# Kernel optimization log

Measured on AMD Instinct MI355X. Metric: run time of the kernel, lower is better.

The kernel has to match this reference:

```python
import jax, jax.numpy as jnp
import numpy as np

D_MODEL = 512
NUM_HEADS = 8
HEAD_DIM = D_MODEL // NUM_HEADS  # 64
EMBEDDING_DIM = 512  # undefined global EmbeddingDim in source -> d_model
EVENT_DIM = 388      # undefined global EventDim in source -> MIDI event vocab
B, T = 2, 2048


def setup_inputs() -> dict:
    key = jax.random.key(0)
    ks = jax.random.split(key, 12)
    sc = 0.02
    v = jax.random.normal(ks[0], (B, T, D_MODEL), jnp.float32)
    k = jax.random.normal(ks[1], (B, T, D_MODEL), jnp.float32)
    q = jax.random.normal(ks[2], (B, T, D_MODEL), jnp.float32)
    mask = jnp.tril(jnp.ones((T, T), jnp.float32))  # causal mask, broadcasts to [H,B,T,T]
    Wq = jax.random.normal(ks[3], (D_MODEL, HEAD_DIM), jnp.float32) * sc
    bq = jnp.zeros((HEAD_DIM,), jnp.float32)
    Wk = jax.random.normal(ks[4], (D_MODEL, HEAD_DIM), jnp.float32) * sc
    bk = jnp.zeros((HEAD_DIM,), jnp.float32)
    Wv = jax.random.normal(ks[5], (D_MODEL, HEAD_DIM), jnp.float32) * sc
    bv = jnp.zeros((HEAD_DIM,), jnp.float32)
    E = jax.random.normal(ks[6], (NUM_HEADS, T, HEAD_DIM), jnp.float32) * sc
    Wo = jax.random.normal(ks[7], (D_MODEL, EMBEDDING_DIM), jnp.float32) * sc
    bo = jnp.zeros((EMBEDDING_DIM,), jnp.float32)
    Wl = jax.random.normal(ks[8], (EMBEDDING_DIM, EVENT_DIM), jnp.float32) * sc
    bl = jnp.zeros((EVENT_DIM,), jnp.float32)
    return {"v": v, "k": k, "q": q, "mask": mask, "Wq": Wq, "bq": bq,
            "Wk": Wk, "bk": bk, "Wv": Wv, "bv": bv, "E": E,
            "Wo": Wo, "bo": bo, "Wl": Wl, "bl": bl}


def _skew(S):
    # S: [H,B,T,T] -> Music-Transformer skew via left-pad, reshape, slice
    H, Bb, Tt, _ = S.shape
    S = jnp.pad(S, ((0, 0), (0, 0), (0, 0), (1, 0)))          # [H,B,T,T+1]
    S = S.reshape(H, Bb, Tt + 1, Tt)                           # [H,B,T+1,T]
    return S[:, :, 1:]                                         # [H,B,T,T]


def reference(v, k, q, mask, Wq, bq, Wk, bk, Wv, bv, E, Wo, bo, Wl, bl):
    # The source applies the SAME Dense per head, so all heads share q/k/v projections
    qh = q @ Wq + bq  # [B,T,hd]
    kh = k @ Wk + bk  # [B,T,hd]
    vh = v @ Wv + bv  # [B,T,hd]
    # relative-position scores per head: Q @ E^T then skew
    S = jnp.einsum('btd,hsd->hbts', qh, E)  # [H,B,T,T]
    S = _skew(S)
    qk = jnp.einsum('btd,bsd->bts', qh, kh)  # [B,T,T], identical across heads
    attn = (qk[None] + S) / np.sqrt(HEAD_DIM)  # [H,B,T,T]
    attn = attn * mask - jnp.asarray(1e10, attn.dtype) * (1.0 - mask)
    score = jax.nn.softmax(attn, axis=-1)
    ctx = jnp.einsum('hbts,bsd->hbtd', score, vh)  # [H,B,T,hd]
    ctx = jnp.transpose(ctx, (1, 2, 0, 3)).reshape(ctx.shape[1], ctx.shape[2], -1)  # [B,T,d_model]
    ctx = jax.nn.relu(ctx @ Wo + bo)  # [B,T,EmbeddingDim]
    logits = ctx @ Wl + bl            # [B,T,EventDim]
    return logits
```

## Files before the change

kernel.cpp:

```cpp
#include <hip/hip_runtime.h>
#include <hip/hip_bf16.h>


#define B_ 2
#define T_ 2048
#define DM_ 512
#define H_ 8
#define HD_ 64
#define ED_ 512
#define EV_ 388
#define BT_ (B_ * T_)

typedef __attribute__((ext_vector_type(8))) short short8;
typedef __attribute__((ext_vector_type(4))) float floatx4;

#define MFMA(a, b, c) __builtin_amdgcn_mfma_f32_16x16x32_bf16((a), (b), (c), 0, 0, 0)

__device__ __forceinline__ float bfs(unsigned short s) {
  union { unsigned int i; float f; } v; v.i = ((unsigned int)s) << 16; return v.f;
}
__device__ __forceinline__ unsigned short f2bf(float f) {
  __hip_bfloat16 h = __float2bfloat16(f);
  union { __hip_bfloat16 h; unsigned short u; } v; v.h = h; return v.u;
}
__device__ __forceinline__ float ldf(const void* p, int i, bool isbf) {
  return isbf ? bfs(((const unsigned short*)p)[i]) : ((const float*)p)[i];
}
__device__ __forceinline__ bool det_bf(const unsigned int* mask) {
  return mask[0] != 0x3F800000u;
}

__global__ __launch_bounds__(256) void prep_kernel(
    const void* __restrict__ E, const void* __restrict__ Wq,
    const void* __restrict__ Wk, const void* __restrict__ Wv,
    const void* __restrict__ Wo, const void* __restrict__ Wl,
    const unsigned int* __restrict__ mask,
    unsigned short* __restrict__ E_c, unsigned short* __restrict__ WqT,
    unsigned short* __restrict__ WkT, unsigned short* __restrict__ WvT,
    unsigned short* __restrict__ WoT, unsigned short* __restrict__ WlT) {
  const bool isbf = det_bf(mask);
  const int tid = threadIdx.x;
  int bi = blockIdx.x;
  if (bi < 1024) {
    const int i0 = (bi * 256 + tid) * 4;
    if (isbf) {
      *(uint2*)&E_c[i0] = *(const uint2*)((const unsigned short*)E + i0);
    } else {
      float4 f = *(const float4*)((const float*)E + i0);
      unsigned short p[4] = {f2bf(f.x), f2bf(f.y), f2bf(f.z), f2bf(f.w)};
      *(uint2*)&E_c[i0] = *(uint2*)p;
    }
    return;
  }
  bi -= 1024;
  const void* src; unsigned short* dst; int N, nb;
  if (bi < 16)       { src = Wq; dst = WqT; N = 64;  nb = bi; }
  else if (bi < 32)  { src = Wk; dst = WkT; N = 64;  nb = bi - 16; }
  else if (bi < 48)  { src = Wv; dst = WvT; N = 64;  nb = bi - 32; }
  else if (bi < 176) { src = Wo; dst = WoT; N = 512; nb = bi - 48; }
  else               { src = Wl; dst = WlT; N = 388; nb = bi - 176; }
  const int n = nb * 4 + (tid >> 6);
  const int k0 = (tid & 63) * 8;
  unsigned short vv[8];
#pragma unroll
  for (int j = 0; j < 8; ++j) {
    if (n >= N) vv[j] = 0;
    else if (isbf) vv[j] = ((const unsigned short*)src)[(size_t)(k0 + j) * N + n];
    else vv[j] = f2bf(((const float*)src)[(size_t)(k0 + j) * N + n]);
  }
  *(uint4*)&dst[(size_t)n * DM_ + k0] = *(uint4*)vv;
}

__global__ __launch_bounds__(256) void gemm_proj(
    const void* __restrict__ xq, const void* __restrict__ xk,
    const void* __restrict__ xv,
    const unsigned short* __restrict__ WqT, const unsigned short* __restrict__ WkT,
    const unsigned short* __restrict__ WvT,
    const void* __restrict__ bq, const void* __restrict__ bk,
    const void* __restrict__ bv, const unsigned int* __restrict__ mask,
    unsigned short* __restrict__ oq, unsigned short* __restrict__ ok,
    unsigned short* __restrict__ ovt) {
  __shared__ __align__(16) short sA[64][72];
  __shared__ __align__(16) short sW[64][72];
  const int sel = blockIdx.y;
  const void* x = (sel == 0) ? xq : (sel == 1) ? xk : xv;
  const unsigned short* WT = (sel == 0) ? WqT : (sel == 1) ? WkT : WvT;
  const void* bias = (sel == 0) ? bq : (sel == 1) ? bk : bv;
  const bool isbf = det_bf(mask);

  const int tid = threadIdx.x;
  const int w = tid >> 6, lane = tid & 63;
  const int q_ = lane >> 4, n_ = lane & 15;
  const int row0 = blockIdx.x * 64;

  floatx4 acc[4];
#pragma unroll
  for (int j = 0; j < 4; ++j) acc[j] = (floatx4){0.f, 0.f, 0.f, 0.f};

  for (int k0 = 0; k0 < DM_; k0 += 64) {
    if (isbf) {
#pragma unroll
      for (int it = 0; it < 2; ++it) {
        int idx = tid + it * 256;
        int rr = idx >> 3, cc = (idx & 7) * 8;
        *(uint4*)&sA[rr][cc] =
            *(const uint4*)((const unsigned short*)x + (size_t)(row0 + rr) * DM_ + k0 + cc);
      }
    } else {
#pragma unroll
      for (int it = 0; it < 4; ++it) {
        int idx = tid + it * 256;
        int rr = idx >> 4, cc = (idx & 15) * 4;
        float4 f = *(const float4*)((const float*)x + (size_t)(row0 + rr) * DM_ + k0 + cc);
        unsigned short p[4] = {f2bf(f.x), f2bf(f.y), f2bf(f.z), f2bf(f.w)};
        *(uint2*)&sA[rr][cc] = *(uint2*)p;
      }
    }
#pragma unroll
    for (int it = 0; it < 2; ++it) {
      int idx = tid + it * 256;
      int rr = idx >> 3, cc = (idx & 7) * 8;
      *(uint4*)&sW[rr][cc] = *(const uint4*)(WT + (size_t)rr * DM_ + k0 + cc);
    }
    __syncthreads();
    short8 a0 = *(const short8*)&sA[16 * w + n_][8 * q_];
    short8 a1 = *(const short8*)&sA[16 * w + n_][32 + 8 * q_];
#pragma unroll
    for (int nb = 0; nb < 4; ++nb) {
      short8 b0 = *(const short8*)&sW[16 * nb + n_][8 * q_];
      short8 b1 = *(const short8*)&sW[16 * nb + n_][32 + 8 * q_];
      acc[nb] = MFMA(a0, b0, acc[nb]);
      acc[nb] = MFMA(a1, b1, acc[nb]);
    }
    __syncthreads();
  }

#pragma unroll
  for (int nb = 0; nb < 4; ++nb) {
    const int col = 16 * nb + n_;
    const float bb = ldf(bias, col, isbf);
#pragma unroll
    for (int r = 0; r < 4; ++r) {
      int row = row0 + 16 * w + 4 * q_ + r;
      unsigned short val = f2bf(acc[nb][r] + bb);
      if (sel < 2) {
        unsigned short* o = (sel == 0) ? oq : ok;
        o[(size_t)row * HD_ + col] = val;
      } else {
        int b = row >> 11, s = row & 2047;
        ovt[(((size_t)(b * HD_ + col)) << 11) + s] = val;
      }
    }
  }
}

__device__ __forceinline__ int pbase_of(int ti) {
  return (ti < 16) ? (ti - 8) * 2 : (ti < 24) ? 16 + (ti - 16) * 3
                                              : 40 + (ti - 24) * 4;
}

__global__ __launch_bounds__(256) void attn_kernel(
    const unsigned short* __restrict__ qh, const unsigned short* __restrict__ kh,
    const unsigned short* __restrict__ vt, const unsigned short* __restrict__ E,
    unsigned short* __restrict__ ctxo, float* __restrict__ pc,
    float* __restrict__ ml) {
  __shared__ __align__(16) short sK[64][72];
  __shared__ __align__(16) short sVT[64][72];
  __shared__ __align__(16) short sP[64][72];

  const int id = blockIdx.x;
  const int hb = id / 80;
  const int rem = id % 80;
  int ti, c, nc;
  if (rem < 8)       { ti = rem;                 c = 0;            nc = 1; }
  else if (rem < 24) { ti = 8 + ((rem - 8) >> 1);  c = (rem - 8) & 1;  nc = 2; }
  else if (rem < 48) { ti = 16 + (rem - 24) / 3;   c = (rem - 24) % 3; nc = 3; }
  else               { ti = 24 + ((rem - 48) >> 2); c = (rem - 48) & 3; nc = 4; }
  const int nsteps = ti + 1;
  const int klo = (c * nsteps) / nc;
  const int khi = ((c + 1) * nsteps) / nc;

  const int h = hb >> 1, b = hb & 1;
  const int t0 = ti * 64;

  const int tid = threadIdx.x;
  const int w = tid >> 6, lane = tid & 63;
  const int q_ = lane >> 4, n_ = lane & 15;

  const int trow = t0 + 16 * w + n_;
  const unsigned short* qp = qh + (((size_t)((b << 11) + trow)) << 6) + (q_ << 3);
  const short8 qa0 = *(const short8*)qp;
  const short8 qa1 = *(const short8*)(qp + 32);

  short8 onesf;
#pragma unroll
  for (int j = 0; j < 8; ++j) onesf[j] = (short)0x3F80;

  floatx4 ctxa[4];
#pragma unroll
  for (int nb = 0; nb < 4; ++nb) ctxa[nb] = (floatx4){0.f, 0.f, 0.f, 0.f};
  floatx4 lacc = (floatx4){0.f, 0.f, 0.f, 0.f};

  const unsigned short* eb = E + ((size_t)h << 17);
  const unsigned short* kbase = kh + (((size_t)(b << 11)) << 6);
  const unsigned short* vbase = vt + (((size_t)(b << 6)) << 11);
  const int rrS = tid >> 3, ccS = (tid & 7) * 8;

  for (int kt = klo; kt < khi; ++kt) {
    const int s0 = kt * 64;
    const int rb = (T_ - 64) + s0 - t0;

    short8 e0[5], e1[5];
#pragma unroll
    for (int f = 0; f < 5; ++f) {
      int gr = rb + 16 * (3 - w + f) + n_;
      if (gr > T_ - 1) gr = T_ - 1;
      const unsigned short* ep = eb + ((size_t)gr << 6) + (q_ << 3);
      e0[f] = *(const short8*)ep;
      e1[f] = *(const short8*)(ep + 32);
    }

    __syncthreads();
#pragma unroll
    for (int it = 0; it < 2; ++it) {
      int rr = rrS + it * 32;
      *(uint4*)&sK[rr][ccS] =
          *(const uint4*)(kbase + (((size_t)(s0 + rr)) << 6) + ccS);
      *(uint4*)&sVT[rr][ccS] =
          *(const uint4*)(vbase + (((size_t)rr) << 11) + s0 + ccS);
    }
    __syncthreads();

    floatx4 qk[4];
#pragma unroll
    for (int nb = 0; nb < 4; ++nb) {
      short8 kb0 = *(const short8*)&sK[16 * nb + n_][8 * q_];
      short8 kb1 = *(const short8*)&sK[16 * nb + n_][32 + 8 * q_];
      qk[nb] = (floatx4){0.f, 0.f, 0.f, 0.f};
      qk[nb] = MFMA(qa0, kb0, qk[nb]);
      qk[nb] = MFMA(qa1, kb1, qk[nb]);
    }
    floatx4 qe[5];
#pragma unroll
    for (int f = 0; f < 5; ++f) {
      qe[f] = (floatx4){0.f, 0.f, 0.f, 0.f};
      qe[f] = MFMA(qa0, e0[f], qe[f]);
      qe[f] = MFMA(qa1, e1[f], qe[f]);
    }

    const bool diag = (kt == ti);
#pragma unroll
    for (int r = 0; r < 4; ++r) {
      const int t = 4 * q_ + r;
      const int ba = ((q_ << 4) | ((n_ - t + 15) & 15)) << 2;
      const int nd = (n_ + t + 1) & 15;
      const bool hi = nd > t;
#pragma unroll
      for (int mb = 0; mb < 4; ++mb) {
        float merged = hi ? qe[mb + 1][r] : qe[mb][r];
        float g = __int_as_float(
            __builtin_amdgcn_ds_bpermute(ba, __float_as_int(merged)));
        float sv = (qk[mb][r] + g) * 0.125f;
        if (diag && (16 * mb + n_ > 16 * w + t)) sv = -1.0e30f;
        sP[16 * w + t][16 * mb + n_] = (short)f2bf(__expf(sv));
      }
    }

    short8 pa0 = *(const short8*)&sP[16 * w + n_][8 * q_];
    short8 pa1 = *(const short8*)&sP[16 * w + n_][32 + 8 * q_];
#pragma unroll
    for (int nb = 0; nb < 4; ++nb) {
      short8 v0 = *(const short8*)&sVT[16 * nb + n_][8 * q_];
      short8 v1 = *(const short8*)&sVT[16 * nb + n_][32 + 8 * q_];
      ctxa[nb] = MFMA(pa0, v0, ctxa[nb]);
      ctxa[nb] = MFMA(pa1, v1, ctxa[nb]);
    }
    lacc = MFMA(pa0, onesf, lacc);
    lacc = MFMA(pa1, onesf, lacc);
  }

  if (nc == 1) {
#pragma unroll
    for (int r = 0; r < 4; ++r) {
      const float inv = 1.0f / lacc[r];
      const int row = t0 + 16 * w + 4 * q_ + r;
      const size_t base = (((size_t)((b << 11) + row)) << 9) + (h << 6) + n_;
#pragma unroll
      for (int nb = 0; nb < 4; ++nb)
        ctxo[base + 16 * nb] = f2bf(ctxa[nb][r] * inv);
    }
  } else {
    const int idx = hb * 72 + pbase_of(ti) + c;
    float* pcb = pc + ((size_t)idx << 12);
    float* mlb = ml + ((size_t)idx << 6);
#pragma unroll
    for (int r = 0; r < 4; ++r) {
      const int row = 16 * w + 4 * q_ + r;
#pragma unroll
      for (int nb = 0; nb < 4; ++nb)
        pcb[(row << 6) + 16 * nb + n_] = ctxa[nb][r];
      if (n_ == 0) mlb[row] = lacc[r];
    }
  }
}

__global__ __launch_bounds__(256) void combine_kernel(
    const float* __restrict__ pc, const float* __restrict__ ml,
    unsigned short* __restrict__ ctxo) {
  const int cb = blockIdx.x;
  const int hb = cb / 24;
  const int ti = 8 + cb % 24;
  const int nc = (ti >> 3) + 1;
  const int h = hb >> 1, b = hb & 1, t0 = ti * 64;
  const int tid = threadIdx.x;
  const int row = tid >> 2, seg = (tid & 3) * 16;
  const int idx0 = hb * 72 + pbase_of(ti);

  float lsum = 0.f;
  float4 a4[4];
#pragma unroll
  for (int j = 0; j < 4; ++j) a4[j] = (float4){0.f, 0.f, 0.f, 0.f};
  for (int c = 0; c < nc; ++c) {
    const int idx = idx0 + c;
    lsum += ml[((size_t)idx << 6) + row];
    const float* cp = pc + ((size_t)idx << 12) + (row << 6) + seg;
#pragma unroll
    for (int j = 0; j < 4; ++j) {
      float4 x = *(const float4*)(cp + 4 * j);
      a4[j].x += x.x; a4[j].y += x.y; a4[j].z += x.z; a4[j].w += x.w;
    }
  }
  const float inv = 1.0f / lsum;
  unsigned short o[16];
#pragma unroll
  for (int j = 0; j < 4; ++j) {
    o[4 * j + 0] = f2bf(a4[j].x * inv);
    o[4 * j + 1] = f2bf(a4[j].y * inv);
    o[4 * j + 2] = f2bf(a4[j].z * inv);
    o[4 * j + 3] = f2bf(a4[j].w * inv);
  }
  unsigned short* dst =
      ctxo + (((size_t)((b << 11) + t0 + row)) << 9) + (h << 6) + seg;
  *(uint4*)dst = *(uint4*)&o[0];
  *(uint4*)(dst + 8) = *(uint4*)&o[8];
}

template <int RELU>
__global__ __launch_bounds__(256) void mlp_mfma(
    const unsigned short* __restrict__ A, const unsigned short* __restrict__ WT,
    const void* __restrict__ bias, unsigned short* __restrict__ outBF,
    void* __restrict__ outD, const unsigned int* __restrict__ mask) {
  __shared__ __align__(16) short sA[64][72];
  __shared__ __align__(16) short sW[64][72];
  const int tid = threadIdx.x;
  const int w = tid >> 6, lane = tid & 63;
  const int q_ = lane >> 4, n_ = lane & 15;
  const int row0 = blockIdx.x * 64;
  const int n0 = blockIdx.y * 64;
  const bool isbf = det_bf(mask);

  floatx4 acc[4];
#pragma unroll
  for (int j = 0; j < 4; ++j) acc[j] = (floatx4){0.f, 0.f, 0.f, 0.f};

  for (int k0 = 0; k0 < DM_; k0 += 64) {
#pragma unroll
    for (int it = 0; it < 2; ++it) {
      int idx = tid + it * 256;
      int rr = idx >> 3, cc = (idx & 7) * 8;
      *(uint4*)&sA[rr][cc] = *(const uint4*)(A + (size_t)(row0 + rr) * DM_ + k0 + cc);
      *(uint4*)&sW[rr][cc] = *(const uint4*)(WT + (size_t)(n0 + rr) * DM_ + k0 + cc);
    }
    __syncthreads();
    short8 a0 = *(const short8*)&sA[16 * w + n_][8 * q_];
    short8 a1 = *(const short8*)&sA[16 * w + n_][32 + 8 * q_];
#pragma unroll
    for (int nb = 0; nb < 4; ++nb) {
      short8 b0 = *(const short8*)&sW[16 * nb + n_][8 * q_];
      short8 b1 = *(const short8*)&sW[16 * nb + n_][32 + 8 * q_];
      acc[nb] = MFMA(a0, b0, acc[nb]);
      acc[nb] = MFMA(a1, b1, acc[nb]);
    }
    __syncthreads();
  }

#pragma unroll
  for (int nb = 0; nb < 4; ++nb) {
    const int col = n0 + 16 * nb + n_;
    float bb = 0.f;
    if (RELU || col < EV_) bb = ldf(bias, col, isbf);
#pragma unroll
    for (int r = 0; r < 4; ++r) {
      const int row = row0 + 16 * w + 4 * q_ + r;
      float v = acc[nb][r] + bb;
      if (RELU) {
        outBF[(size_t)row * ED_ + col] = f2bf(fmaxf(v, 0.f));
      } else if (col < EV_) {
        if (isbf) ((unsigned short*)outD)[(size_t)row * EV_ + col] = f2bf(v);
        else      ((float*)outD)[(size_t)row * EV_ + col] = v;
      }
    }
  }
}

extern "C" void kernel_launch(void* const* d_in, const int* in_sizes, int n_in,
                              void* d_out, int out_size, void* d_ws, size_t ws_size,
                              hipStream_t stream) {
  const void* v  = d_in[0];
  const void* k  = d_in[1];
  const void* q  = d_in[2];
  const unsigned int* mask = (const unsigned int*)d_in[3];
  const void* Wq = d_in[4];
  const void* bq = d_in[5];
  const void* Wk = d_in[6];
  const void* bk = d_in[7];
  const void* Wv = d_in[8];
  const void* bv = d_in[9];
  const void* E  = d_in[10];
  const void* Wo = d_in[11];
  const void* bo = d_in[12];
  const void* Wl = d_in[13];
  const void* bl = d_in[14];

  char* p = (char*)d_ws;
  unsigned short* E_c  = (unsigned short*)p; p += (size_t)H_ * T_ * HD_ * 2;
  unsigned short* qhb  = (unsigned short*)p; p += (size_t)BT_ * HD_ * 2;
  unsigned short* khb  = (unsigned short*)p; p += (size_t)BT_ * HD_ * 2;
  unsigned short* vtb  = (unsigned short*)p; p += (size_t)BT_ * HD_ * 2;
  unsigned short* WqT  = (unsigned short*)p; p += (size_t)HD_ * DM_ * 2;
  unsigned short* WkT  = (unsigned short*)p; p += (size_t)HD_ * DM_ * 2;
  unsigned short* WvT  = (unsigned short*)p; p += (size_t)HD_ * DM_ * 2;
  unsigned short* WoT  = (unsigned short*)p; p += (size_t)ED_ * DM_ * 2;
  unsigned short* WlT  = (unsigned short*)p; p += (size_t)448 * DM_ * 2;
  unsigned short* ctxb = (unsigned short*)p; p += (size_t)BT_ * DM_ * 2;
  unsigned short* h1b  = (unsigned short*)p; p += (size_t)BT_ * ED_ * 2;
  float* pc = (float*)p; p += (size_t)16 * 72 * 4096 * 4;
  float* ml = (float*)p; p += (size_t)16 * 72 * 64 * 4;

  prep_kernel<<<dim3(1312), 256, 0, stream>>>(
      E, Wq, Wk, Wv, Wo, Wl, mask, E_c, WqT, WkT, WvT, WoT, WlT);
  gemm_proj<<<dim3(BT_ / 64, 3), 256, 0, stream>>>(
      q, k, v, WqT, WkT, WvT, bq, bk, bv, mask, qhb, khb, vtb);
  attn_kernel<<<dim3(1280), 256, 0, stream>>>(qhb, khb, vtb, E_c, ctxb, pc, ml);
  combine_kernel<<<dim3(384), 256, 0, stream>>>(pc, ml, ctxb);
  mlp_mfma<1><<<dim3(BT_ / 64, ED_ / 64), 256, 0, stream>>>(
      ctxb, WoT, bo, h1b, nullptr, mask);
  mlp_mfma<0><<<dim3(BT_ / 64, 448 / 64), 256, 0, stream>>>(
      h1b, WlT, bl, nullptr, d_out, mask);
}
```

Measured before the change: 225.1 us.

## Register-prefetch next K/V/E tiles, XOR-swizzle LDS, and raise MFMA priority

```diff
diff --git a/kernel.cpp b/kernel.cpp
--- a/kernel.cpp
+++ b/kernel.cpp
@@ -164,9 +164,9 @@
     const unsigned short* __restrict__ vt, const unsigned short* __restrict__ E,
     unsigned short* __restrict__ ctxo, float* __restrict__ pc,
     float* __restrict__ ml) {
-  __shared__ __align__(16) short sK[64][72];
-  __shared__ __align__(16) short sVT[64][72];
-  __shared__ __align__(16) short sP[64][72];
+  __shared__ __align__(16) short sK[64][64];
+  __shared__ __align__(16) short sVT[64][64];
+  __shared__ __align__(16) short sP[64][64];
 
   const int id = blockIdx.x;
   const int hb = id / 80;
@@ -205,12 +205,21 @@
   const unsigned short* kbase = kh + (((size_t)(b << 11)) << 6);
   const unsigned short* vbase = vt + (((size_t)(b << 6)) << 11);
   const int rrS = tid >> 3, ccS = (tid & 7) * 8;
-
-  for (int kt = klo; kt < khi; ++kt) {
-    const int s0 = kt * 64;
+  const int scS = (((tid & 7) ^ (rrS & 7)) << 3);
+  const int c0s = ((q_ ^ (n_ & 7)) << 3);
+  const int c1s = (((q_ | 4) ^ (n_ & 7)) << 3);
+
+  uint4 kreg[2], vreg[2];
+  short8 e0[5], e1[5];
+  {
+    const int s0 = klo * 64;
+#pragma unroll
+    for (int it = 0; it < 2; ++it) {
+      const int rr = rrS + it * 32;
+      kreg[it] = *(const uint4*)(kbase + (((size_t)(s0 + rr)) << 6) + ccS);
+      vreg[it] = *(const uint4*)(vbase + (((size_t)rr) << 11) + s0 + ccS);
+    }
     const int rb = (T_ - 64) + s0 - t0;
-
-    short8 e0[5], e1[5];
 #pragma unroll
     for (int f = 0; f < 5; ++f) {
       int gr = rb + 16 * (3 - w + f) + n_;
@@ -219,23 +228,33 @@
       e0[f] = *(const short8*)ep;
       e1[f] = *(const short8*)(ep + 32);
     }
-
-    __syncthreads();
-#pragma unroll
-    for (int it = 0; it < 2; ++it) {
-      int rr = rrS + it * 32;
-      *(uint4*)&sK[rr][ccS] =
-          *(const uint4*)(kbase + (((size_t)(s0 + rr)) << 6) + ccS);
-      *(uint4*)&sVT[rr][ccS] =
-          *(const uint4*)(vbase + (((size_t)rr) << 11) + s0 + ccS);
+  }
+
+  for (int kt = klo; kt < khi; ++kt) {
+    __syncthreads();
+
+    *(uint4*)&sK[rrS][scS] = kreg[0];
+    *(uint4*)&sK[rrS + 32][scS] = kreg[1];
+    *(uint4*)&sVT[rrS][scS] = vreg[0];
+    *(uint4*)&sVT[rrS + 32][scS] = vreg[1];
+
+    if (kt + 1 < khi) {
+      const int s0n = (kt + 1) * 64;
+#pragma unroll
+      for (int it = 0; it < 2; ++it) {
+        const int rr = rrS + it * 32;
+        kreg[it] = *(const uint4*)(kbase + (((size_t)(s0n + rr)) << 6) + ccS);
+        vreg[it] = *(const uint4*)(vbase + (((size_t)rr) << 11) + s0n + ccS);
+      }
     }
     __syncthreads();
 
     floatx4 qk[4];
+    __builtin_amdgcn_s_setprio(1);
 #pragma unroll
     for (int nb = 0; nb < 4; ++nb) {
-      short8 kb0 = *(const short8*)&sK[16 * nb + n_][8 * q_];
-      short8 kb1 = *(const short8*)&sK[16 * nb + n_][32 + 8 * q_];
+      short8 kb0 = *(const short8*)&sK[16 * nb + n_][c0s];
+      short8 kb1 = *(const short8*)&sK[16 * nb + n_][c1s];
       qk[nb] = (floatx4){0.f, 0.f, 0.f, 0.f};
       qk[nb] = MFMA(qa0, kb0, qk[nb]);
       qk[nb] = MFMA(qa1, kb1, qk[nb]);
@@ -246,6 +265,19 @@
       qe[f] = (floatx4){0.f, 0.f, 0.f, 0.f};
       qe[f] = MFMA(qa0, e0[f], qe[f]);
       qe[f] = MFMA(qa1, e1[f], qe[f]);
+    }
+    __builtin_amdgcn_s_setprio(0);
+
+    if (kt + 1 < khi) {
+      const int rbn = (T_ - 64) + (kt + 1) * 64 - t0;
+#pragma unroll
+      for (int f = 0; f < 5; ++f) {
+        int gr = rbn + 16 * (3 - w + f) + n_;
+        if (gr > T_ - 1) gr = T_ - 1;
+        const unsigned short* ep = eb + ((size_t)gr << 6) + (q_ << 3);
+        e0[f] = *(const short8*)ep;
+        e1[f] = *(const short8*)(ep + 32);
+      }
     }
 
     const bool diag = (kt == ti);
@@ -255,28 +287,32 @@
       const int ba = ((q_ << 4) | ((n_ - t + 15) & 15)) << 2;
       const int nd = (n_ + t + 1) & 15;
       const bool hi = nd > t;
+      const int swr = (t & 7) << 3;
 #pragma unroll
       for (int mb = 0; mb < 4; ++mb) {
         float merged = hi ? qe[mb + 1][r] : qe[mb][r];
         float g = __int_as_float(
             __builtin_amdgcn_ds_bpermute(ba, __float_as_int(merged)));
-        float sv = (qk[mb][r] + g) * 0.125f;
+        float sv = qk[mb][r] + g;
         if (diag && (16 * mb + n_ > 16 * w + t)) sv = -1.0e30f;
-        sP[16 * w + t][16 * mb + n_] = (short)f2bf(__expf(sv));
-      }
-    }
-
-    short8 pa0 = *(const short8*)&sP[16 * w + n_][8 * q_];
-    short8 pa1 = *(const short8*)&sP[16 * w + n_][32 + 8 * q_];
+        sP[16 * w + t][(16 * mb + n_) ^ swr] =
+            (short)f2bf(exp2f(sv * 0.18033688011f));
+      }
+    }
+
+    short8 pa0 = *(const short8*)&sP[16 * w + n_][c0s];
+    short8 pa1 = *(const short8*)&sP[16 * w + n_][c1s];
+    __builtin_amdgcn_s_setprio(1);
 #pragma unroll
     for (int nb = 0; nb < 4; ++nb) {
-      short8 v0 = *(const short8*)&sVT[16 * nb + n_][8 * q_];
-      short8 v1 = *(const short8*)&sVT[16 * nb + n_][32 + 8 * q_];
+      short8 v0 = *(const short8*)&sVT[16 * nb + n_][c0s];
+      short8 v1 = *(const short8*)&sVT[16 * nb + n_][c1s];
       ctxa[nb] = MFMA(pa0, v0, ctxa[nb]);
       ctxa[nb] = MFMA(pa1, v1, ctxa[nb]);
     }
     lacc = MFMA(pa0, onesf, lacc);
     lacc = MFMA(pa1, onesf, lacc);
+    __builtin_amdgcn_s_setprio(0);
   }
 
   if (nc == 1) {
```

Measured after the change: 256.1 us. +13.8%, slower.

## Double-buffer K/V via direct global-to-LDS loads with swizzled LDS and rebalanced splits

Applied to the files above, without the earlier changes.

```diff
diff --git a/kernel.cpp b/kernel.cpp
--- a/kernel.cpp
+++ b/kernel.cpp
@@ -28,6 +28,11 @@
 }
 __device__ __forceinline__ bool det_bf(const unsigned int* mask) {
   return mask[0] != 0x3F800000u;
+}
+__device__ __forceinline__ void gl_lds16(const unsigned short* g, void* l) {
+  __builtin_amdgcn_global_load_lds(
+      (const __attribute__((address_space(1))) void*)g,
+      (__attribute__((address_space(3))) void*)l, 16, 0, 0);
 }
 
 __global__ __launch_bounds__(256) void prep_kernel(
@@ -155,27 +160,25 @@
 }
 
 __device__ __forceinline__ int pbase_of(int ti) {
-  return (ti < 16) ? (ti - 8) * 2 : (ti < 24) ? 16 + (ti - 16) * 3
-                                              : 40 + (ti - 24) * 4;
-}
-
-__global__ __launch_bounds__(256) void attn_kernel(
+  return (ti < 22) ? (ti - 11) * 2 : 22 + (ti - 22) * 3;
+}
+
+__global__ __launch_bounds__(256, 4) void attn_kernel(
     const unsigned short* __restrict__ qh, const unsigned short* __restrict__ kh,
     const unsigned short* __restrict__ vt, const unsigned short* __restrict__ E,
     unsigned short* __restrict__ ctxo, float* __restrict__ pc,
     float* __restrict__ ml) {
-  __shared__ __align__(16) short sK[64][72];
-  __shared__ __align__(16) short sVT[64][72];
-  __shared__ __align__(16) short sP[64][72];
+  __shared__ __align__(16) short sK[2][64][64];
+  __shared__ __align__(16) short sVT[2][64][64];
+  __shared__ __align__(16) short sP[64][64];
 
   const int id = blockIdx.x;
-  const int hb = id / 80;
-  const int rem = id % 80;
+  const int hb = id / 63;
+  const int rem = id % 63;
   int ti, c, nc;
-  if (rem < 8)       { ti = rem;                 c = 0;            nc = 1; }
-  else if (rem < 24) { ti = 8 + ((rem - 8) >> 1);  c = (rem - 8) & 1;  nc = 2; }
-  else if (rem < 48) { ti = 16 + (rem - 24) / 3;   c = (rem - 24) % 3; nc = 3; }
-  else               { ti = 24 + ((rem - 48) >> 2); c = (rem - 48) & 3; nc = 4; }
+  if (rem < 11)      { ti = rem;                  c = 0;              nc = 1; }
+  else if (rem < 33) { ti = 11 + ((rem - 11) >> 1); c = (rem - 11) & 1; nc = 2; }
+  else               { ti = 22 + (rem - 33) / 3;    c = (rem - 33) % 3; nc = 3; }
   const int nsteps = ti + 1;
   const int klo = (c * nsteps) / nc;
   const int khi = ((c + 1) * nsteps) / nc;
@@ -204,12 +207,41 @@
   const unsigned short* eb = E + ((size_t)h << 17);
   const unsigned short* kbase = kh + (((size_t)(b << 11)) << 6);
   const unsigned short* vbase = vt + (((size_t)(b << 6)) << 11);
-  const int rrS = tid >> 3, ccS = (tid & 7) * 8;
+
+  const int lrow = lane >> 3;
+  const int lchunk = ((lane & 7) ^ lrow) << 3;
+  const int rK0 = 8 * w + lrow;
+  const int c0s = ((q_ ^ (n_ & 7)) << 3);
+  const int c1s = (((q_ | 4) ^ (n_ & 7)) << 3);
+
+#define STAGE(bufsel, s0v)                                                     \
+  {                                                                            \
+    void* dK = (void*)&sK[bufsel][8 * w][0];                                   \
+    void* dV = (void*)&sVT[bufsel][8 * w][0];                                  \
+    const unsigned short* gK =                                                 \
+        kbase + (((size_t)((s0v) + rK0)) << 6) + lchunk;                       \
+    const unsigned short* gV =                                                 \
+        vbase + (((size_t)rK0) << 11) + (s0v) + lchunk;                        \
+    gl_lds16(gK, dK);                                                          \
+    gl_lds16(gK + (32 << 6), (void*)((short*)dK + 32 * 64));                   \
+    gl_lds16(gV, dV);                                                          \
+    gl_lds16(gV + (32 << 11), (void*)((short*)dV + 32 * 64));                  \
+  }
+
+  STAGE(0, klo * 64);
 
   for (int kt = klo; kt < khi; ++kt) {
+    const int cur = (kt - klo) & 1;
     const int s0 = kt * 64;
+
+    asm volatile("s_waitcnt vmcnt(0)" ::: "memory");
+    __builtin_amdgcn_sched_barrier(0);
+    __builtin_amdgcn_s_barrier();
+    __builtin_amdgcn_sched_barrier(0);
+
+    if (kt + 1 < khi) STAGE(cur ^ 1, s0 + 64);
+
     const int rb = (T_ - 64) + s0 - t0;
-
     short8 e0[5], e1[5];
 #pragma unroll
     for (int f = 0; f < 5; ++f) {
@@ -220,22 +252,12 @@
       e1[f] = *(const short8*)(ep + 32);
     }
 
-    __syncthreads();
-#pragma unroll
-    for (int it = 0; it < 2; ++it) {
-      int rr = rrS + it * 32;
-      *(uint4*)&sK[rr][ccS] =
-          *(const uint4*)(kbase + (((size_t)(s0 + rr)) << 6) + ccS);
-      *(uint4*)&sVT[rr][ccS] =
-          *(const uint4*)(vbase + (((size_t)rr) << 11) + s0 + ccS);
-    }
-    __syncthreads();
-
     floatx4 qk[4];
+    __builtin_amdgcn_s_setprio(1);
 #pragma unroll
     for (int nb = 0; nb < 4; ++nb) {
-      short8 kb0 = *(const short8*)&sK[16 * nb + n_][8 * q_];
-      short8 kb1 = *(const short8*)&sK[16 * nb + n_][32 + 8 * q_];
+      short8 kb0 = *(const short8*)&sK[cur][16 * nb + n_][c0s];
+      short8 kb1 = *(const short8*)&sK[cur][16 * nb + n_][c1s];
       qk[nb] = (floatx4){0.f, 0.f, 0.f, 0.f};
       qk[nb] = MFMA(qa0, kb0, qk[nb]);
       qk[nb] = MFMA(qa1, kb1, qk[nb]);
@@ -247,6 +269,7 @@
       qe[f] = MFMA(qa0, e0[f], qe[f]);
       qe[f] = MFMA(qa1, e1[f], qe[f]);
     }
+    __builtin_amdgcn_s_setprio(0);
 
     const bool diag = (kt == ti);
 #pragma unroll
@@ -255,29 +278,34 @@
       const int ba = ((q_ << 4) | ((n_ - t + 15) & 15)) << 2;
       const int nd = (n_ + t + 1) & 15;
       const bool hi = nd > t;
+      const int swr = (t & 7) << 3;
 #pragma unroll
       for (int mb = 0; mb < 4; ++mb) {
         float merged = hi ? qe[mb + 1][r] : qe[mb][r];
         float g = __int_as_float(
             __builtin_amdgcn_ds_bpermute(ba, __float_as_int(merged)));
-        float sv = (qk[mb][r] + g) * 0.125f;
+        float sv = qk[mb][r] + g;
         if (diag && (16 * mb + n_ > 16 * w + t)) sv = -1.0e30f;
-        sP[16 * w + t][16 * mb + n_] = (short)f2bf(__expf(sv));
+        sP[16 * w + t][(16 * mb + n_) ^ swr] =
+            (short)f2bf(exp2f(sv * 0.18033688011f));
       }
     }
 
-    short8 pa0 = *(const short8*)&sP[16 * w + n_][8 * q_];
-    short8 pa1 = *(const short8*)&sP[16 * w + n_][32 + 8 * q_];
+    short8 pa0 = *(const short8*)&sP[16 * w + n_][c0s];
+    short8 pa1 = *(const short8*)&sP[16 * w + n_][c1s];
+    __builtin_amdgcn_s_setprio(1);
 #pragma unroll
     for (int nb = 0; nb < 4; ++nb) {
-      short8 v0 = *(const short8*)&sVT[16 * nb + n_][8 * q_];
-      short8 v1 = *(const short8*)&sVT[16 * nb + n_][32 + 8 * q_];
+      short8 v0 = *(const short8*)&sVT[cur][16 * nb + n_][c0s];
+      short8 v1 = *(const short8*)&sVT[cur][16 * nb + n_][c1s];
       ctxa[nb] = MFMA(pa0, v0, ctxa[nb]);
       ctxa[nb] = MFMA(pa1, v1, ctxa[nb]);
     }
     lacc = MFMA(pa0, onesf, lacc);
     lacc = MFMA(pa1, onesf, lacc);
-  }
+    __builtin_amdgcn_s_setprio(0);
+  }
+#undef STAGE
 
   if (nc == 1) {
 #pragma unroll
@@ -290,7 +318,7 @@
         ctxo[base + 16 * nb] = f2bf(ctxa[nb][r] * inv);
     }
   } else {
-    const int idx = hb * 72 + pbase_of(ti) + c;
+    const int idx = hb * 52 + pbase_of(ti) + c;
     float* pcb = pc + ((size_t)idx << 12);
     float* mlb = ml + ((size_t)idx << 6);
 #pragma unroll
@@ -308,13 +336,13 @@
     const float* __restrict__ pc, const float* __restrict__ ml,
     unsigned short* __restrict__ ctxo) {
   const int cb = blockIdx.x;
-  const int hb = cb / 24;
-  const int ti = 8 + cb % 24;
-  const int nc = (ti >> 3) + 1;
+  const int hb = cb / 21;
+  const int ti = 11 + cb % 21;
+  const int nc = (ti < 22) ? 2 : 3;
   const int h = hb >> 1, b = hb & 1, t0 = ti * 64;
   const int tid = threadIdx.x;
   const int row = tid >> 2, seg = (tid & 3) * 16;
-  const int idx0 = hb * 72 + pbase_of(ti);
+  const int idx0 = hb * 52 + pbase_of(ti);
 
   float lsum = 0.f;
   float4 a4[4];
@@ -434,15 +462,15 @@
   unsigned short* WlT  = (unsigned short*)p; p += (size_t)448 * DM_ * 2;
   unsigned short* ctxb = (unsigned short*)p; p += (size_t)BT_ * DM_ * 2;
   unsigned short* h1b  = (unsigned short*)p; p += (size_t)BT_ * ED_ * 2;
-  float* pc = (float*)p; p += (size_t)16 * 72 * 4096 * 4;
-  float* ml = (float*)p; p += (size_t)16 * 72 * 64 * 4;
+  float* pc = (float*)p; p += (size_t)16 * 52 * 4096 * 4;
+  float* ml = (float*)p; p += (size_t)16 * 52 * 64 * 4;
 
   prep_kernel<<<dim3(1312), 256, 0, stream>>>(
       E, Wq, Wk, Wv, Wo, Wl, mask, E_c, WqT, WkT, WvT, WoT, WlT);
   gemm_proj<<<dim3(BT_ / 64, 3), 256, 0, stream>>>(
       q, k, v, WqT, WkT, WvT, bq, bk, bv, mask, qhb, khb, vtb);
-  attn_kernel<<<dim3(1280), 256, 0, stream>>>(qhb, khb, vtb, E_c, ctxb, pc, ml);
-  combine_kernel<<<dim3(384), 256, 0, stream>>>(pc, ml, ctxb);
+  attn_kernel<<<dim3(1008), 256, 0, stream>>>(qhb, khb, vtb, E_c, ctxb, pc, ml);
+  combine_kernel<<<dim3(336), 256, 0, stream>>>(pc, ml, ctxb);
   mlp_mfma<1><<<dim3(BT_ / 64, ED_ / 64), 256, 0, stream>>>(
       ctxb, WoT, bo, h1b, nullptr, mask);
   mlp_mfma<0><<<dim3(BT_ / 64, 448 / 64), 256, 0, stream>>>(
```

After: 217.9 us. 1.03x faster.
